# Kernel optimization log

Measured on AMD Instinct MI355X. Metric: run time of the kernel, lower is better.

The kernel has to match this reference:

```python
import jax, jax.numpy as jnp
import numpy as np

T, B = 64, 32
V, E, H = 32000, 1024, 1024


def setup_inputs() -> dict:
    key = jax.random.key(0)
    ks = jax.random.split(key, 8)
    return {
        "target_tokens": jax.random.randint(ks[0], (T, B), 0, V),
        "ground_truth": jax.random.randint(ks[1], (T, B), 0, V),
        "embedding": jax.random.normal(ks[2], (V, E), jnp.float32) * 0.02,
        "W_ih": jax.random.normal(ks[3], (E, 4 * H), jnp.float32) / np.sqrt(E),
        "W_hh": jax.random.normal(ks[4], (H, 4 * H), jnp.float32) / np.sqrt(H),
        "b": jnp.zeros((4 * H,), jnp.float32),
        "W_out": jax.random.normal(ks[5], (H, V), jnp.float32) / np.sqrt(H),
        "b_out": jnp.zeros((V,), jnp.float32),
    }


def _lstm_logits(emb, W_ih, W_hh, b, W_out, b_out):
    # emb: [T, B, E] time-major; initial state (H_C=None) -> zeros
    Bsz = emb.shape[1]
    h0 = jnp.zeros((Bsz, W_hh.shape[0]), emb.dtype)
    c0 = jnp.zeros_like(h0)
    # precompute input projection for all timesteps in one GEMM
    x_proj = jnp.einsum('tbe,eg->tbg', emb, W_ih) + b  # [T, B, 4H]

    def step(carry, xg):
        h, c = carry
        gates = xg + h @ W_hh  # [B, 4H]
        i, f, g, o = jnp.split(gates, 4, axis=-1)
        c = jax.nn.sigmoid(f) * c + jax.nn.sigmoid(i) * jnp.tanh(g)
        h = jax.nn.sigmoid(o) * jnp.tanh(c)
        return (h, c), h

    (_, _), hs = jax.lax.scan(step, (h0, c0), x_proj)  # hs: [T, B, H]
    logits = jnp.einsum('tbh,hv->tbv', hs, W_out) + b_out  # [T, B, V]
    return logits


def reference(target_tokens, ground_truth, embedding, W_ih, W_hh, b, W_out, b_out):
    emb = embedding[target_tokens]  # [T, B, E]
    logits = _lstm_logits(emb, W_ih, W_hh, b, W_out, b_out)
    logits2d = logits.reshape(-1, logits.shape[-1])  # [T*B, V]
    gt = ground_truth.reshape(-1)  # [T*B]
    logp = jax.nn.log_softmax(logits2d, axis=-1)
    nll = -jnp.take_along_axis(logp, gt[:, None], axis=1)[:, 0]
    return jnp.mean(nll)
```

## Files before the change

kernel.cpp:

```cpp
#include <hip/hip_runtime.h>
#include <hip/hip_bf16.h>

typedef unsigned short u16;
typedef unsigned char u8;
typedef unsigned long long ull;
typedef __attribute__((ext_vector_type(8))) short bf16x8;
typedef __attribute__((ext_vector_type(4))) float f32x4;
typedef __attribute__((ext_vector_type(4))) int i32x4;
typedef __attribute__((ext_vector_type(8))) int i32x8;

#define NSLICE 500

__device__ __forceinline__ u16 f2bf(float x){
  unsigned b = __float_as_uint(x);
  return (u16)((b + 0x7FFFu + ((b>>16)&1u)) >> 16);
}
__device__ __forceinline__ float sigm(float x){ return 1.f/(1.f+__expf(-x)); }

__device__ __forceinline__ void gload_lds16(const void* g, void* l){
  __builtin_amdgcn_global_load_lds(
      (const __attribute__((address_space(1))) unsigned int*)g,
      (__attribute__((address_space(3))) unsigned int*)l, 16, 0, 0);
}
#define SWZ(row, kb) ((kb) ^ (((row)&7)<<4))

template<int OFF>
__device__ __forceinline__ i32x4 gload16_coh(const char* p){
  i32x4 d;
  asm volatile("global_load_dwordx4 %0, %1, off offset:%2 sc0 sc1"
               : "=v"(d) : "v"(p), "n"(OFF) : "memory");
  return d;
}

__device__ __forceinline__ f32x4 mfma_f8(i32x8 a, i32x8 b, f32x4 c){
  asm("v_mfma_f32_16x16x128_f8f6f4 %0, %1, %2, %0" : "+v"(c) : "v"(a), "v"(b));
  return c;
}

__device__ __forceinline__ void load_tile64(
    const float* __restrict__ in, int N, int nb, int kb, float (*tile)[65])
{
  const int t = threadIdx.x;
#pragma unroll
  for (int i=0;i<4;++i){
    int idx = i*256 + t;
    int k = idx>>4, n4 = idx&15;
    const float4 v = *(const float4*)&in[(size_t)(kb+k)*N + nb + n4*4];
    tile[k][n4*4+0]=v.x; tile[k][n4*4+1]=v.y; tile[k][n4*4+2]=v.z; tile[k][n4*4+3]=v.w;
  }
  __syncthreads();
}

__global__ __launch_bounds__(256) void prep_kernel(
    const float* __restrict__ Wih, const float* __restrict__ Whh,
    const int* __restrict__ tok, const float* __restrict__ emb,
    u16* __restrict__ WihT, u16* __restrict__ WhhT,
    u16* __restrict__ embg, float* __restrict__ zbuf, float* __restrict__ out0)
{
  __shared__ float tile[64][65];
  const int b = blockIdx.x;
  const int t = threadIdx.x;
  if (b < 2048){
    const int i = (b < 1024) ? b : b - 1024;
    const float* in = (b < 1024) ? Wih : Whh;
    u16* out = (b < 1024) ? WihT : WhhT;
    const int nb = (i&63)*64, kb = (i>>6)*64;
    load_tile64(in, 4096, nb, kb, tile);
#pragma unroll
    for (int ii=0;ii<2;++ii){
      int idx = ii*256 + t;
      int n = idx>>3, k8 = idx&7;
      u16 tmp[8];
#pragma unroll
      for (int jj=0;jj<8;++jj) tmp[jj] = f2bf(tile[k8*8+jj][n]);
      *(ulonglong2*)&out[(size_t)(nb+n)*1024 + kb + k8*8] = *(ulonglong2*)tmp;
    }
  } else if (b < 4096){
    const int r = b - 2048;
    const int trow = tok[r];
    const float4 v = *(const float4*)(emb + (size_t)trow*1024 + t*4);
    ull o = (ull)f2bf(v.x) | ((ull)f2bf(v.y)<<16) | ((ull)f2bf(v.z)<<32) | ((ull)f2bf(v.w)<<48);
    *(ull*)(embg + (size_t)r*1024 + t*4) = o;
  } else {
    const int i = (b - 4096)*256 + t;
    if (i < 65792) zbuf[i] = 0.f;
    if (i == 0) out0[0] = 0.f;
  }
}

__device__ __forceinline__ void gemm_tile_128(
    const u16* __restrict__ A, const u16* __restrict__ BT,
    int rowbase, int colbase, u16* As, u16* Bs, f32x4 (&acc)[4][4])
{
  const int tid = threadIdx.x;
  const int lane = tid & 63;
  const int wm = (tid>>6)>>1, wn = (tid>>6)&1;
#pragma unroll
  for (int m=0;m<4;++m)
#pragma unroll
    for (int n=0;n<4;++n) acc[m][n] = (f32x4){0.f,0.f,0.f,0.f};

  for (int kb = 0; kb < 1024; kb += 64){
    __syncthreads();
#pragma unroll
    for (int i=0;i<4;++i){
      const int row = i*32 + (tid>>3);
      const int kf  = (tid&7)*16;
      gload_lds16((const char*)(A  + (size_t)(rowbase+row)*1024 + kb) + SWZ(row,kf),
                  (char*)As + (i*256+tid)*16);
      gload_lds16((const char*)(BT + (size_t)(colbase+row)*1024 + kb) + SWZ(row,kf),
                  (char*)Bs + (i*256+tid)*16);
    }
    __syncthreads();
#pragma unroll
    for (int ks=0;ks<2;++ks){
      bf16x8 af[4], bfr[4];
      const int kbyte = ks*64 + (lane>>4)*16;
#pragma unroll
      for (int m=0;m<4;++m){
        const int row = wm*64 + m*16 + (lane&15);
        af[m] = *(const bf16x8*)((const char*)As + row*128 + SWZ(row,kbyte));
      }
#pragma unroll
      for (int n=0;n<4;++n){
        const int col = wn*64 + n*16 + (lane&15);
        bfr[n] = *(const bf16x8*)((const char*)Bs + col*128 + SWZ(col,kbyte));
      }
#pragma unroll
      for (int m=0;m<4;++m)
#pragma unroll
        for (int n=0;n<4;++n)
          acc[m][n] = __builtin_amdgcn_mfma_f32_16x16x32_bf16(af[m], bfr[n], acc[m][n], 0,0,0);
    }
  }
}

__global__ __launch_bounds__(256,2) void xproj_gemm(
    const u16* __restrict__ Aemb, const u16* __restrict__ WihT,
    const float* __restrict__ bias, float* __restrict__ xgP)
{
  __shared__ u16 As[8192], Bs[8192];
  const int fb = blockIdx.x;
  const int g = (fb&7)*64 + (fb>>3);
  const int ct = g>>4, rt = g&15;
  const int rowbase = rt*128, colbase = ct*128;
  const int tid = threadIdx.x, lane = tid&63;
  const int wm = (tid>>6)>>1, wn = (tid>>6)&1;
  f32x4 acc[4][4];
  gemm_tile_128(Aemb, WihT, rowbase, colbase, As, Bs, acc);
  float bv[4];
#pragma unroll
  for (int n=0;n<4;++n) bv[n] = bias[colbase + wn*64 + n*16 + (lane&15)];
#pragma unroll
  for (int m=0;m<4;++m)
#pragma unroll
    for (int n=0;n<4;++n)
#pragma unroll
      for (int r=0;r<4;++r){
        const int row = rowbase + wm*64 + m*16 + (lane>>4)*4 + r;
        const int col = colbase + wn*64 + n*16 + (lane&15);
        const int tt = row>>5, b = row&31;
        const int q = col>>10, hcol = col&1023;
        xgP[(size_t)(((tt*256 + (hcol>>2))*32 + b)*16 + (hcol&3)*4 + q)] = acc[m][n][r] + bv[n];
      }
}

__global__ __launch_bounds__(256,1) void lstm_persistent(
    const u16* __restrict__ WhhT, const float* __restrict__ xgP,
    u16* __restrict__ hb0, u16* __restrict__ hb1, u8* __restrict__ hsf8,
    unsigned* __restrict__ bar,
    const float* __restrict__ Wout, u8* __restrict__ WoutT8)
{
  __shared__ float red[4*32*16];
  __shared__ float tile[64][65];
  const int cb = blockIdx.x;
  const int tid = threadIdx.x, lane = tid&63, w = tid>>6;
  const int f = lane & 15;
  const int kfrag = (lane>>4)*8;
  const int gcol = cb*4 + (f&3) + 1024*(f>>2);
  const int bb = tid>>2, j = tid&3;
  const int w8 = w*8;

  bf16x8 wreg[8];
#pragma unroll
  for (int i=0;i<8;++i)
    wreg[i] = *(const bf16x8*)(WhhT + (size_t)gcol*1024 + (w8+i)*32 + kfrag);

  float creg = 0.f;
  float4 x4 = {0.f,0.f,0.f,0.f};
  if (tid < 128)
    x4 = *(const float4*)(xgP + ((size_t)0*256 + cb)*512 + bb*16 + j*4);

  for (int t=0; t<64; ++t){
    const u16* hin = (t&1) ? hb1 : hb0;
    u16*      hout = (t&1) ? hb0 : hb1;

    const char* p0 = (const char*)(hin + (size_t)f*1024 + w8*32 + kfrag);
    const char* p1 = p0 + 32768;
    i32x4 h0[8], h1[8];
    h0[0]=gload16_coh<  0>(p0); h0[1]=gload16_coh< 64>(p0);
    h0[2]=gload16_coh<128>(p0); h0[3]=gload16_coh<192>(p0);
    h0[4]=gload16_coh<256>(p0); h0[5]=gload16_coh<320>(p0);
    h0[6]=gload16_coh<384>(p0); h0[7]=gload16_coh<448>(p0);
    h1[0]=gload16_coh<  0>(p1); h1[1]=gload16_coh< 64>(p1);
    h1[2]=gload16_coh<128>(p1); h1[3]=gload16_coh<192>(p1);
    h1[4]=gload16_coh<256>(p1); h1[5]=gload16_coh<320>(p1);
    h1[6]=gload16_coh<384>(p1); h1[7]=gload16_coh<448>(p1);
    asm volatile("s_waitcnt vmcnt(0)" ::: "memory");
    __builtin_amdgcn_sched_barrier(0);

    f32x4 acc0 = (f32x4){0.f,0.f,0.f,0.f};
    f32x4 acc1 = (f32x4){0.f,0.f,0.f,0.f};
#pragma unroll
    for (int i=0;i<8;++i){
      acc0 = __builtin_amdgcn_mfma_f32_16x16x32_bf16(
                 __builtin_bit_cast(bf16x8, h0[i]), wreg[i], acc0, 0,0,0);
      acc1 = __builtin_amdgcn_mfma_f32_16x16x32_bf16(
                 __builtin_bit_cast(bf16x8, h1[i]), wreg[i], acc1, 0,0,0);
    }
#pragma unroll
    for (int r=0;r<4;++r){
      red[w*512 + ((lane>>4)*4 + r)*16 + f]      = acc0[r];
      red[w*512 + (16 + (lane>>4)*4 + r)*16 + f] = acc1[r];
    }
    __syncthreads();
    unsigned hu = 0, fb8 = 0;
    if (tid < 128){
      float g4[4];
#pragma unroll
      for (int q=0;q<4;++q){
        const int ff = j + 4*q;
        g4[q] = red[0*512 + bb*16 + ff] + red[1*512 + bb*16 + ff]
              + red[2*512 + bb*16 + ff] + red[3*512 + bb*16 + ff];
      }
      g4[0] += x4.x; g4[1] += x4.y; g4[2] += x4.z; g4[3] += x4.w;
      const float iv = sigm(g4[0]), fv = sigm(g4[1]);
      const float gv = tanhf(g4[2]), ov = sigm(g4[3]);
      const float cn = fv*creg + iv*gv;
      const float hv = ov*tanhf(cn);
      creg = cn;
      hu = (unsigned)f2bf(hv);
      fb8 = __builtin_amdgcn_cvt_pk_fp8_f32(hv, 0.f, 0, 0) & 0xffu;
    }
    const unsigned v1 = __shfl_down(hu, 1, 64);
    const unsigned v2 = __shfl_down(hu, 2, 64);
    const unsigned v3 = __shfl_down(hu, 3, 64);
    const ull p = (ull)hu | ((ull)v1<<16) | ((ull)v2<<32) | ((ull)v3<<48);
    const unsigned f1 = __shfl_down(fb8, 1, 64);
    const unsigned f2 = __shfl_down(fb8, 2, 64);
    const unsigned f3 = __shfl_down(fb8, 3, 64);
    const unsigned pf = fb8 | (f1<<8) | (f2<<16) | (f3<<24);
    if (tid < 128 && j == 0){
      __hip_atomic_store((ull*)&hout[bb*1024 + cb*4], p,
                         __ATOMIC_RELAXED, __HIP_MEMORY_SCOPE_AGENT);
    }
    const int tile_id = (t>>1)*256 + cb;
    if (t < 63){
      __syncthreads();
      if (tid == 0)
        __hip_atomic_fetch_add(&bar[(cb & 7)*32], 1u,
                               __ATOMIC_RELAXED, __HIP_MEMORY_SCOPE_AGENT);
      if (tid < 128 && j == 0)
        *(unsigned*)&hsf8[(size_t)t*32768 + bb*1024 + cb*4] = pf;
      if (tid < 128)
        x4 = *(const float4*)(xgP + ((size_t)(t+1)*256 + cb)*512 + bb*16 + j*4);
      if (tile_id < 8000){
        const int nb = (tile_id % 500)*64, kb = (tile_id / 500)*64;
        if ((t & 1) == 0){
#pragma unroll
          for (int i=0;i<4;++i){
            int idx = i*256 + tid;
            int k = idx>>4, n4 = idx&15;
            const float4 v = *(const float4*)&Wout[(size_t)(kb+k)*32000 + nb + n4*4];
            tile[k][n4*4+0]=v.x; tile[k][n4*4+1]=v.y;
            tile[k][n4*4+2]=v.z; tile[k][n4*4+3]=v.w;
          }
        } else {
#pragma unroll
          for (int i=0;i<2;++i){
            int idx = i*256 + tid;
            int n = idx>>3, k8 = idx&7;
            float v0=tile[k8*8+0][n], s1=tile[k8*8+1][n], s2=tile[k8*8+2][n], s3=tile[k8*8+3][n];
            float v4=tile[k8*8+4][n], s5=tile[k8*8+5][n], s6=tile[k8*8+6][n], s7=tile[k8*8+7][n];
            unsigned w0 = __builtin_amdgcn_cvt_pk_fp8_f32(v0, s1, 0, 0);
            w0 = __builtin_amdgcn_cvt_pk_fp8_f32(s2, s3, w0, 1);
            unsigned w1 = __builtin_amdgcn_cvt_pk_fp8_f32(v4, s5, 0, 0);
            w1 = __builtin_amdgcn_cvt_pk_fp8_f32(s6, s7, w1, 1);
            *(ull*)&WoutT8[(size_t)(nb+n)*1024 + kb + k8*8] = (ull)w0 | ((ull)w1<<32);
          }
        }
      }
      if (tid == 0){
        const unsigned target = (unsigned)(t+1)*32u;
        for (;;){
          bool ok = true;
#pragma unroll
          for (int i=0;i<8;++i)
            ok &= (__hip_atomic_load(&bar[i*32], __ATOMIC_RELAXED,
                                     __HIP_MEMORY_SCOPE_AGENT) >= target);
          if (ok) break;
          __builtin_amdgcn_s_sleep(2);
        }
        asm volatile("" ::: "memory");
      }
      __syncthreads();
    } else {
      if (tid < 128 && j == 0)
        *(unsigned*)&hsf8[(size_t)63*32768 + bb*1024 + cb*4] = pf;
      if (tile_id < 8000){
        const int nb = (tile_id % 500)*64, kb = (tile_id / 500)*64;
#pragma unroll
        for (int i=0;i<2;++i){
          int idx = i*256 + tid;
          int n = idx>>3, k8 = idx&7;
          float v0=tile[k8*8+0][n], s1=tile[k8*8+1][n], s2=tile[k8*8+2][n], s3=tile[k8*8+3][n];
          float v4=tile[k8*8+4][n], s5=tile[k8*8+5][n], s6=tile[k8*8+6][n], s7=tile[k8*8+7][n];
          unsigned w0 = __builtin_amdgcn_cvt_pk_fp8_f32(v0, s1, 0, 0);
          w0 = __builtin_amdgcn_cvt_pk_fp8_f32(s2, s3, w0, 1);
          unsigned w1 = __builtin_amdgcn_cvt_pk_fp8_f32(v4, s5, 0, 0);
          w1 = __builtin_amdgcn_cvt_pk_fp8_f32(s6, s7, w1, 1);
          *(ull*)&WoutT8[(size_t)(nb+n)*1024 + kb + k8*8] = (ull)w0 | ((ull)w1<<32);
        }
      }
    }
  }
}

__global__ __launch_bounds__(256,2) void logits_gemm_lse(
    const u8* __restrict__ hs8, const u8* __restrict__ WoutT8,
    const float* __restrict__ bout, const int* __restrict__ gt,
    float* __restrict__ partm, float* __restrict__ parts, float* __restrict__ gtl)
{
  __shared__ u8 As8[16384], Bs8[16384];
  __shared__ int gts[128];
  const int fb = blockIdx.x;
  const int g = (fb&7)*500 + (fb>>3);
  const int vt = g>>4, rt = g&15;
  const int rowbase = rt*128, colbase = vt*128;
  const int tid = threadIdx.x, lane = tid&63;
  const int wm = (tid>>6)>>1, wn = (tid>>6)&1;
  if (tid < 128) gts[tid] = gt[rowbase + tid];
  f32x4 acc[4][4];
#pragma unroll
  for (int m=0;m<4;++m)
#pragma unroll
    for (int n=0;n<4;++n) acc[m][n] = (f32x4){0.f,0.f,0.f,0.f};

  for (int kb = 0; kb < 8; ++kb){
    __syncthreads();
#pragma unroll
    for (int i=0;i<4;++i){
      const int row = i*32 + (tid>>3);
      const int kf  = (tid&7)*16;
      gload_lds16((const char*)(hs8    + (size_t)(rowbase+row)*1024 + kb*128) + SWZ(row,kf),
                  (char*)As8 + (i*256+tid)*16);
      gload_lds16((const char*)(WoutT8 + (size_t)(colbase+row)*1024 + kb*128) + SWZ(row,kf),
                  (char*)Bs8 + (i*256+tid)*16);
    }
    __syncthreads();
    const int kbyte = (lane>>4)*32;
    i32x8 af[4], bfr[4];
#pragma unroll
    for (int m=0;m<4;++m){
      const int row = wm*64 + m*16 + (lane&15);
      union { i32x8 v8; i32x4 v4[2]; } u;
      u.v4[0] = *(const i32x4*)(As8 + row*128 + SWZ(row, kbyte));
      u.v4[1] = *(const i32x4*)(As8 + row*128 + SWZ(row, kbyte+16));
      af[m] = u.v8;
    }
#pragma unroll
    for (int n=0;n<4;++n){
      const int col = wn*64 + n*16 + (lane&15);
      union { i32x8 v8; i32x4 v4[2]; } u;
      u.v4[0] = *(const i32x4*)(Bs8 + col*128 + SWZ(col, kbyte));
      u.v4[1] = *(const i32x4*)(Bs8 + col*128 + SWZ(col, kbyte+16));
      bfr[n] = u.v8;
    }
#pragma unroll
    for (int m=0;m<4;++m)
#pragma unroll
      for (int n=0;n<4;++n)
        acc[m][n] = mfma_f8(af[m], bfr[n], acc[m][n]);
  }

  float bv[4];
#pragma unroll
  for (int n=0;n<4;++n) bv[n] = bout[colbase + wn*64 + n*16 + (lane&15)];
#pragma unroll
  for (int m=0;m<4;++m)
#pragma unroll
    for (int n=0;n<4;++n)
#pragma unroll
      for (int r=0;r<4;++r) acc[m][n][r] += bv[n];
  float rm[4][4], rs[4][4];
#pragma unroll
  for (int m=0;m<4;++m)
#pragma unroll
    for (int r=0;r<4;++r){
      float mx = fmaxf(fmaxf(acc[m][0][r],acc[m][1][r]), fmaxf(acc[m][2][r],acc[m][3][r]));
      mx = fmaxf(mx, __shfl_xor(mx,1,16));
      mx = fmaxf(mx, __shfl_xor(mx,2,16));
      mx = fmaxf(mx, __shfl_xor(mx,4,16));
      mx = fmaxf(mx, __shfl_xor(mx,8,16));
      float sv = __expf(acc[m][0][r]-mx) + __expf(acc[m][1][r]-mx)
               + __expf(acc[m][2][r]-mx) + __expf(acc[m][3][r]-mx);
      sv += __shfl_xor(sv,1,16);
      sv += __shfl_xor(sv,2,16);
      sv += __shfl_xor(sv,4,16);
      sv += __shfl_xor(sv,8,16);
      rm[m][r]=mx; rs[m][r]=sv;
    }
  const int slice = vt*2 + wn;
  if ((lane&15)==0){
#pragma unroll
    for (int m=0;m<4;++m)
#pragma unroll
      for (int r=0;r<4;++r){
        const int rloc = wm*64 + m*16 + (lane>>4)*4 + r;
        partm[(size_t)slice*2048 + rowbase + rloc] = rm[m][r];
        parts[(size_t)slice*2048 + rowbase + rloc] = rs[m][r];
      }
  }
#pragma unroll
  for (int m=0;m<4;++m)
#pragma unroll
    for (int r=0;r<4;++r){
      const int rloc = wm*64 + m*16 + (lane>>4)*4 + r;
      const int gg = gts[rloc] - colbase - wn*64;
      if (gg >= 0 && gg < 64 && (gg&15)==(lane&15)){
        const int n = gg>>4;
        const float val = (n==0)?acc[m][0][r] : (n==1)?acc[m][1][r]
                        : (n==2)?acc[m][2][r] : acc[m][3][r];
        gtl[rowbase+rloc] = val;
      }
    }
}

__global__ __launch_bounds__(256) void lse_finalize2(
    const float* __restrict__ partm, const float* __restrict__ parts,
    const float* __restrict__ gtl, float* __restrict__ out)
{
  __shared__ float red[4];
  const int r = blockIdx.x*256 + threadIdx.x;
  float m = -1e30f;
  for (int i=0;i<NSLICE;++i) m = fmaxf(m, partm[(size_t)i*2048 + r]);
  float s = 0.f;
  for (int i=0;i<NSLICE;++i) s += parts[(size_t)i*2048 + r]*__expf(partm[(size_t)i*2048 + r]-m);
  float v = (m + logf(s) - gtl[r]) * (1.0f/2048.0f);
#pragma unroll
  for (int off=32;off>=1;off>>=1) v += __shfl_down(v, off, 64);
  if ((threadIdx.x&63)==0) red[threadIdx.x>>6]=v;
  __syncthreads();
  if (threadIdx.x==0) atomicAdd(out, red[0]+red[1]+red[2]+red[3]);
}

extern "C" void kernel_launch(void* const* d_in, const int* in_sizes, int n_in,
                              void* d_out, int out_size, void* d_ws, size_t ws_size,
                              hipStream_t stream)
{
  const int*   tok  = (const int*)d_in[0];
  const int*   gt   = (const int*)d_in[1];
  const float* emb  = (const float*)d_in[2];
  const float* Wih  = (const float*)d_in[3];
  const float* Whh  = (const float*)d_in[4];
  const float* bias = (const float*)d_in[5];
  const float* Wout = (const float*)d_in[6];
  const float* bout = (const float*)d_in[7];
  float* out = (float*)d_out;

  char* base = (char*)d_ws;
  u8*    WoutT8 = (u8*)base;            base += 32768000;
  u16*   WihT  = (u16*)base;            base += 8388608;
  u16*   WhhT  = (u16*)base;            base += 8388608;
  u16*   embg  = (u16*)base;            base += 4194304;
  float* xgP   = (float*)base;          base += 33554432;
  u8*    hsf8  = (u8*)base;             base += 2097152;
  float* cbuf  = (float*)base;          base += 131072;
  u16*   hb0   = (u16*)base;            base += 65536;
  u16*   hb1   = (u16*)base;            base += 65536;
  unsigned* bar = (unsigned*)base;      base += 1024;
  float* partm = (float*)base;          base += 4096000;
  float* parts = (float*)base;          base += 4096000;
  float* gtl   = (float*)base;          base += 8192;

  prep_kernel<<<4353, 256, 0, stream>>>(Wih, Whh, tok, emb,
                                        WihT, WhhT, embg, cbuf, out);

  xproj_gemm<<<512, 256, 0, stream>>>(embg, WihT, bias, xgP);

  lstm_persistent<<<256, 256, 0, stream>>>(WhhT, xgP, hb0, hb1, hsf8, bar,
                                           Wout, WoutT8);

  logits_gemm_lse<<<4000, 256, 0, stream>>>(hsf8, WoutT8, bout, gt, partm, parts, gtl);
  lse_finalize2<<<8, 256, 0, stream>>>(partm, parts, gtl, out);
}
```

Baseline: 529.1 us.

## Move W_out fp8 transpose from LSTM barrier gaps into xproj GEMM launch

The W_out transpose-to-fp8 work, previously spread across the per-timestep barrier waits of the persistent LSTM kernel, is moved into extra blocks (8000 tiles) appended to the input-projection GEMM launch. This shortens each sequential LSTM step, which sits on the critical path, at the cost of adding about 128MB of fp32 reads plus the fp8 writes to a kernel that runs before the recurrence. Shared memory is reused between the GEMM and transpose roles through a union buffer.

```diff
diff --git a/kernel.cpp b/kernel.cpp
--- a/kernel.cpp
+++ b/kernel.cpp
@@ -135,44 +135,72 @@
   }
 }
 
-__global__ __launch_bounds__(256,2) void xproj_gemm(
+__global__ __launch_bounds__(256,2) void xproj_plus(
     const u16* __restrict__ Aemb, const u16* __restrict__ WihT,
-    const float* __restrict__ bias, float* __restrict__ xgP)
-{
-  __shared__ u16 As[8192], Bs[8192];
+    const float* __restrict__ bias, float* __restrict__ xgP,
+    const float* __restrict__ Wout, u8* __restrict__ WoutT8)
+{
+  __shared__ ull smem8[4096];
   const int fb = blockIdx.x;
-  const int g = (fb&7)*64 + (fb>>3);
-  const int ct = g>>4, rt = g&15;
-  const int rowbase = rt*128, colbase = ct*128;
-  const int tid = threadIdx.x, lane = tid&63;
-  const int wm = (tid>>6)>>1, wn = (tid>>6)&1;
-  f32x4 acc[4][4];
-  gemm_tile_128(Aemb, WihT, rowbase, colbase, As, Bs, acc);
-  float bv[4];
-#pragma unroll
-  for (int n=0;n<4;++n) bv[n] = bias[colbase + wn*64 + n*16 + (lane&15)];
-#pragma unroll
-  for (int m=0;m<4;++m)
-#pragma unroll
-    for (int n=0;n<4;++n)
-#pragma unroll
-      for (int r=0;r<4;++r){
-        const int row = rowbase + wm*64 + m*16 + (lane>>4)*4 + r;
-        const int col = colbase + wn*64 + n*16 + (lane&15);
-        const int tt = row>>5, b = row&31;
-        const int q = col>>10, hcol = col&1023;
-        xgP[(size_t)(((tt*256 + (hcol>>2))*32 + b)*16 + (hcol&3)*4 + q)] = acc[m][n][r] + bv[n];
-      }
+  const int tid = threadIdx.x;
+  if (fb < 512){
+    u16* As = (u16*)smem8;
+    u16* Bs = As + 8192;
+    const int g = (fb&7)*64 + (fb>>3);
+    const int ct = g>>4, rt = g&15;
+    const int rowbase = rt*128, colbase = ct*128;
+    const int lane = tid&63;
+    const int wm = (tid>>6)>>1, wn = (tid>>6)&1;
+    f32x4 acc[4][4];
+    gemm_tile_128(Aemb, WihT, rowbase, colbase, As, Bs, acc);
+    float bv[4];
+#pragma unroll
+    for (int n=0;n<4;++n) bv[n] = bias[colbase + wn*64 + n*16 + (lane&15)];
+#pragma unroll
+    for (int m=0;m<4;++m)
+#pragma unroll
+      for (int n=0;n<4;++n)
+#pragma unroll
+        for (int r=0;r<4;++r){
+          const int row = rowbase + wm*64 + m*16 + (lane>>4)*4 + r;
+          const int col = colbase + wn*64 + n*16 + (lane&15);
+          const int tt = row>>5, b = row&31;
+          const int q = col>>10, hcol = col&1023;
+          xgP[(size_t)(((tt*256 + (hcol>>2))*32 + b)*16 + (hcol&3)*4 + q)] = acc[m][n][r] + bv[n];
+        }
+  } else {
+    float (*tile)[65] = (float(*)[65])smem8;
+    const int tile_id = fb - 512;
+    const int nb = (tile_id % 500)*64, kb = (tile_id / 500)*64;
+#pragma unroll
+    for (int i=0;i<4;++i){
+      int idx = i*256 + tid;
+      int k = idx>>4, n4 = idx&15;
+      const float4 v = *(const float4*)&Wout[(size_t)(kb+k)*32000 + nb + n4*4];
+      tile[k][n4*4+0]=v.x; tile[k][n4*4+1]=v.y; tile[k][n4*4+2]=v.z; tile[k][n4*4+3]=v.w;
+    }
+    __syncthreads();
+#pragma unroll
+    for (int i=0;i<2;++i){
+      int idx = i*256 + tid;
+      int n = idx>>3, k8 = idx&7;
+      float v0=tile[k8*8+0][n], s1=tile[k8*8+1][n], s2=tile[k8*8+2][n], s3=tile[k8*8+3][n];
+      float v4=tile[k8*8+4][n], s5=tile[k8*8+5][n], s6=tile[k8*8+6][n], s7=tile[k8*8+7][n];
+      unsigned w0 = __builtin_amdgcn_cvt_pk_fp8_f32(v0, s1, 0, 0);
+      w0 = __builtin_amdgcn_cvt_pk_fp8_f32(s2, s3, w0, 1);
+      unsigned w1 = __builtin_amdgcn_cvt_pk_fp8_f32(v4, s5, 0, 0);
+      w1 = __builtin_amdgcn_cvt_pk_fp8_f32(s6, s7, w1, 1);
+      *(ull*)&WoutT8[(size_t)(nb+n)*1024 + kb + k8*8] = (ull)w0 | ((ull)w1<<32);
+    }
+  }
 }
 
 __global__ __launch_bounds__(256,1) void lstm_persistent(
     const u16* __restrict__ WhhT, const float* __restrict__ xgP,
     u16* __restrict__ hb0, u16* __restrict__ hb1, u8* __restrict__ hsf8,
-    unsigned* __restrict__ bar,
-    const float* __restrict__ Wout, u8* __restrict__ WoutT8)
+    unsigned* __restrict__ bar)
 {
   __shared__ float red[4*32*16];
-  __shared__ float tile[64][65];
   const int cb = blockIdx.x;
   const int tid = threadIdx.x, lane = tid&63, w = tid>>6;
   const int f = lane & 15;
@@ -254,7 +282,6 @@
       __hip_atomic_store((ull*)&hout[bb*1024 + cb*4], p,
                          __ATOMIC_RELAXED, __HIP_MEMORY_SCOPE_AGENT);
     }
-    const int tile_id = (t>>1)*256 + cb;
     if (t < 63){
       __syncthreads();
       if (tid == 0)
@@ -264,32 +291,6 @@
         *(unsigned*)&hsf8[(size_t)t*32768 + bb*1024 + cb*4] = pf;
       if (tid < 128)
         x4 = *(const float4*)(xgP + ((size_t)(t+1)*256 + cb)*512 + bb*16 + j*4);
-      if (tile_id < 8000){
-        const int nb = (tile_id % 500)*64, kb = (tile_id / 500)*64;
-        if ((t & 1) == 0){
-#pragma unroll
-          for (int i=0;i<4;++i){
-            int idx = i*256 + tid;
-            int k = idx>>4, n4 = idx&15;
-            const float4 v = *(const float4*)&Wout[(size_t)(kb+k)*32000 + nb + n4*4];
-            tile[k][n4*4+0]=v.x; tile[k][n4*4+1]=v.y;
-            tile[k][n4*4+2]=v.z; tile[k][n4*4+3]=v.w;
-          }
-        } else {
-#pragma unroll
-          for (int i=0;i<2;++i){
-            int idx = i*256 + tid;
-            int n = idx>>3, k8 = idx&7;
-            float v0=tile[k8*8+0][n], s1=tile[k8*8+1][n], s2=tile[k8*8+2][n], s3=tile[k8*8+3][n];
-            float v4=tile[k8*8+4][n], s5=tile[k8*8+5][n], s6=tile[k8*8+6][n], s7=tile[k8*8+7][n];
-            unsigned w0 = __builtin_amdgcn_cvt_pk_fp8_f32(v0, s1, 0, 0);
-            w0 = __builtin_amdgcn_cvt_pk_fp8_f32(s2, s3, w0, 1);
-            unsigned w1 = __builtin_amdgcn_cvt_pk_fp8_f32(v4, s5, 0, 0);
-            w1 = __builtin_amdgcn_cvt_pk_fp8_f32(s6, s7, w1, 1);
-            *(ull*)&WoutT8[(size_t)(nb+n)*1024 + kb + k8*8] = (ull)w0 | ((ull)w1<<32);
-          }
-        }
-      }
       if (tid == 0){
         const unsigned target = (unsigned)(t+1)*32u;
         for (;;){
@@ -307,21 +308,6 @@
     } else {
       if (tid < 128 && j == 0)
         *(unsigned*)&hsf8[(size_t)63*32768 + bb*1024 + cb*4] = pf;
-      if (tile_id < 8000){
-        const int nb = (tile_id % 500)*64, kb = (tile_id / 500)*64;
-#pragma unroll
-        for (int i=0;i<2;++i){
-          int idx = i*256 + tid;
-          int n = idx>>3, k8 = idx&7;
-          float v0=tile[k8*8+0][n], s1=tile[k8*8+1][n], s2=tile[k8*8+2][n], s3=tile[k8*8+3][n];
-          float v4=tile[k8*8+4][n], s5=tile[k8*8+5][n], s6=tile[k8*8+6][n], s7=tile[k8*8+7][n];
-          unsigned w0 = __builtin_amdgcn_cvt_pk_fp8_f32(v0, s1, 0, 0);
-          w0 = __builtin_amdgcn_cvt_pk_fp8_f32(s2, s3, w0, 1);
-          unsigned w1 = __builtin_amdgcn_cvt_pk_fp8_f32(v4, s5, 0, 0);
-          w1 = __builtin_amdgcn_cvt_pk_fp8_f32(s6, s7, w1, 1);
-          *(ull*)&WoutT8[(size_t)(nb+n)*1024 + kb + k8*8] = (ull)w0 | ((ull)w1<<32);
-        }
-      }
     }
   }
 }
@@ -486,10 +472,9 @@
   prep_kernel<<<4353, 256, 0, stream>>>(Wih, Whh, tok, emb,
                                         WihT, WhhT, embg, cbuf, out);
 
-  xproj_gemm<<<512, 256, 0, stream>>>(embg, WihT, bias, xgP);
-
-  lstm_persistent<<<256, 256, 0, stream>>>(WhhT, xgP, hb0, hb1, hsf8, bar,
-                                           Wout, WoutT8);
+  xproj_plus<<<8512, 256, 0, stream>>>(embg, WihT, bias, xgP, Wout, WoutT8);
+
+  lstm_persistent<<<256, 256, 0, stream>>>(WhhT, xgP, hb0, hb1, hsf8, bar);
 
   logits_gemm_lse<<<4000, 256, 0, stream>>>(hsf8, WoutT8, bout, gt, partm, parts, gtl);
   lse_finalize2<<<8, 256, 0, stream>>>(partm, parts, gtl, out);
```

Result: no change. 539.0 us (+1.9%).
